# Optimization experiments

Measured on AMD Instinct MI355X. Metric: run time of the kernel, lower is better.

Reference implementation:

```python
import jax, jax.numpy as jnp
import numpy as np

N = 20000      # total nodes
E = 320000     # edges (before self loops)
B = 8          # graphs in batch
F_IN = 100
HID = 256
HEADS = 4
DIMS = [(256, 256), (256, 128), (128, 64), (64, 32)]  # (in_dim, out_dim) per level
NEG_SLOPE = 0.2
LN_EPS = 1e-5


def _glorot(k, shape):
    fan = shape[0] + shape[-1]
    return jax.random.normal(k, shape, jnp.float32) * jnp.sqrt(2.0 / fan)


def setup_inputs() -> dict:
    key = jax.random.key(0)
    ks = jax.random.split(key, 32)
    inp = {}
    inp["x"] = jax.random.normal(ks[0], (N, F_IN), jnp.float32)
    inp["edge_index"] = jax.random.randint(ks[1], (2, E), 0, N)
    inp["batch"] = jnp.sort(jax.random.randint(ks[2], (N,), 0, B))
    inp["W_in"] = _glorot(ks[3], (F_IN, HID))
    inp["b_in"] = jnp.zeros((HID,), jnp.float32)
    i = 4
    for l, (di, do) in enumerate(DIMS):
        inp[f"W{l}"] = _glorot(ks[i], (di, HEADS * do)); i += 1
        inp[f"as{l}"] = _glorot(ks[i], (HEADS, do)); i += 1
        inp[f"ad{l}"] = _glorot(ks[i], (HEADS, do)); i += 1
        inp[f"b{l}"] = jnp.zeros((do,), jnp.float32)
        inp[f"g{l}"] = jnp.ones((do,), jnp.float32)
        inp[f"be{l}"] = jnp.zeros((do,), jnp.float32)
    inp["W_out"] = _glorot(ks[i], (DIMS[-1][1], 1))
    inp["b_out"] = jnp.zeros((1,), jnp.float32)
    return inp


def _gat(x, src, dst, W, a_s, a_d, b):
    # PyG GATConv, heads=HEADS, concat=False (head mean), bias after mean
    h = (x @ W).reshape(N, HEADS, -1)              # [N,H,C]
    al_s = (h * a_s).sum(-1)                        # [N,H]
    al_d = (h * a_d).sum(-1)                        # [N,H]
    e = jax.nn.leaky_relu(al_s[src] + al_d[dst], NEG_SLOPE)  # [Etot,H]
    m = jax.ops.segment_max(e, dst, num_segments=N)
    m = jnp.where(jnp.isfinite(m), m, 0.0)
    ex = jnp.exp(e - m[dst])
    den = jax.ops.segment_sum(ex, dst, num_segments=N)
    alpha = ex / (den[dst] + 1e-16)                 # segment softmax over incoming edges
    out = jax.ops.segment_sum(alpha[:, :, None] * h[src], dst, num_segments=N)
    return out.mean(axis=1) + b                     # [N,C]


def _ln(x, g, b):
    mu = x.mean(-1, keepdims=True)
    var = ((x - mu) ** 2).mean(-1, keepdims=True)
    return (x - mu) * jax.lax.rsqrt(var + LN_EPS) * g + b


def _forward(x, edge_index, batch, W_in, b_in, level_params, W_out, b_out):
    loop = jnp.arange(N)
    src = jnp.concatenate([edge_index[0], loop])    # add self loops (GATConv default)
    dst = jnp.concatenate([edge_index[1], loop])
    h = jax.nn.relu(x @ W_in + b_in)
    for (di, do), (W, a_s, a_d, b, g, be) in zip(DIMS, level_params):
        out = _gat(h, src, dst, W, a_s, a_d, b)
        out = jax.nn.relu(out)
        out = _ln(out, g, be)
        # dropout is identity in eval mode
        if di == do:
            out = out + h
        h = out
    cnt = jax.ops.segment_sum(jnp.ones((N,), h.dtype), batch, num_segments=B)
    pooled = jax.ops.segment_sum(h, batch, num_segments=B) / jnp.maximum(cnt, 1.0)[:, None]
    return (pooled @ W_out + b_out)[:, 0]           # [B]


def reference(x, edge_index, batch, W_in, b_in,
              W0, as0, ad0, b0, g0, be0,
              W1, as1, ad1, b1, g1, be1,
              W2, as2, ad2, b2, g2, be2,
              W3, as3, ad3, b3, g3, be3,
              W_out, b_out):
    level_params = [
        (W0, as0, ad0, b0, g0, be0),
        (W1, as1, ad1, b1, g1, be1),
        (W2, as2, ad2, b2, g2, be2),
        (W3, as3, ad3, b3, g3, be3),
    ]
    return _forward(x, edge_index, batch, W_in, b_in, level_params, W_out, b_out)
```

## Files before the change

kernel.cpp:

```cpp
#include <hip/hip_runtime.h>
#include <hip/hip_bf16.h>
#include <cstdint>

constexpr int NN   = 20000;
constexpr int NE   = 320000;
constexpr int ETOT = NE + NN;
constexpr int BG   = 8;
constexpr int FIN  = 100;
constexpr int HID  = 256;
constexpr int H    = 4;
constexpr float SLOPE  = 0.2f;
constexpr float LN_EPS = 1e-5f;

#define DEVFN __device__ __forceinline__

typedef __bf16 bf16x8 __attribute__((ext_vector_type(8)));
typedef float  f32x4  __attribute__((ext_vector_type(4)));
typedef float  f32x2  __attribute__((ext_vector_type(2)));

DEVFN float lrelu(float v) { return v > 0.f ? v : SLOPE * v; }
DEVFN ushort f2bf(float f) {
    unsigned u = __float_as_uint(f);
    return (ushort)((u + 0x7fffu + ((u >> 16) & 1u)) >> 16);
}
DEVFN float bf_lo(unsigned u) { return __uint_as_float(u << 16); }
DEVFN float bf_hi(unsigned u) { return __uint_as_float(u & 0xffff0000u); }
DEVFN float bf2f(unsigned u) { return __uint_as_float(u << 16); }

__global__ void zero_u32(uint32_t* __restrict__ p, int n) {
    int i = blockIdx.x * blockDim.x + threadIdx.x;
    if (i < n) p[i] = 0u;
}

__global__ void count_deg(const int* __restrict__ ei, int* __restrict__ deg) {
    int k = blockIdx.x * blockDim.x + threadIdx.x;
    if (k >= ETOT) return;
    int d = (k < NE) ? ei[NE + k] : (k - NE);
    atomicAdd(&deg[d], 1);
}

__global__ void scan_kernel(const int* __restrict__ deg, int* __restrict__ rowptr) {
    __shared__ int buf[1024];
    int carry = 0;
    for (int base = 0; base < NN; base += 1024) {
        int i = base + threadIdx.x;
        int v = (i < NN) ? deg[i] : 0;
        buf[threadIdx.x] = v;
        __syncthreads();
        for (int off = 1; off < 1024; off <<= 1) {
            int t = (threadIdx.x >= off) ? buf[threadIdx.x - off] : 0;
            __syncthreads();
            buf[threadIdx.x] += t;
            __syncthreads();
        }
        int incl = buf[threadIdx.x];
        if (i < NN) rowptr[i] = carry + incl - v;
        int total = buf[1023];
        __syncthreads();
        carry += total;
    }
    if (threadIdx.x == 0) rowptr[NN] = carry;
}

__global__ void scatter_edges(const int* __restrict__ ei, const int* __restrict__ rowptr,
                              int* __restrict__ fill, int* __restrict__ esrc) {
    int k = blockIdx.x * blockDim.x + threadIdx.x;
    if (k >= ETOT) return;
    int s, d;
    if (k < NE) { s = ei[k]; d = ei[NE + k]; }
    else        { s = k - NE; d = k - NE; }
    int pos = rowptr[d] + atomicAdd(&fill[d], 1);
    esrc[pos] = s;
}

constexpr int CXN  = NN * 128;
constexpr int CWI  = 256 * 128;
constexpr int CW0  = 1024 * 256;
constexpr int CW1  = 512 * 256;
constexpr int CW2  = 256 * 128;
constexpr int CW3  = 128 * 64;
constexpr int CTOT = CXN + CWI + CW0 + CW1 + CW2 + CW3;

__global__ void conv_all(const float* __restrict__ x, const float* __restrict__ Wi,
                         const float* __restrict__ W0, const float* __restrict__ W1,
                         const float* __restrict__ W2, const float* __restrict__ W3,
                         ushort* __restrict__ xpad, ushort* __restrict__ wti,
                         ushort* __restrict__ wt0, ushort* __restrict__ wt1,
                         ushort* __restrict__ wt2, ushort* __restrict__ wt3) {
    int id = blockIdx.x * blockDim.x + threadIdx.x;
    if (id < CXN) {
        int n = id >> 7, k = id & 127;
        xpad[id] = (k < FIN) ? f2bf(x[(size_t)n * FIN + k]) : (ushort)0;
        return;
    }
    id -= CXN;
    if (id < CWI) { int n = id / 128, k = id - n * 128;
        wti[id] = (k < FIN) ? f2bf(Wi[(size_t)k * 256 + n]) : (ushort)0; return; }
    id -= CWI;
    if (id < CW0) { int n = id / 256, k = id - n * 256;
        wt0[id] = f2bf(W0[(size_t)k * 1024 + n]); return; }
    id -= CW0;
    if (id < CW1) { int n = id / 256, k = id - n * 256;
        wt1[id] = f2bf(W1[(size_t)k * 512 + n]); return; }
    id -= CW1;
    if (id < CW2) { int n = id / 128, k = id - n * 128;
        wt2[id] = f2bf(W2[(size_t)k * 256 + n]); return; }
    id -= CW2;
    if (id < CW3) { int n = id / 64, k = id - n * 64;
        wt3[id] = f2bf(W3[(size_t)k * 128 + n]); return; }
}

template <int K, int NC, bool BR, bool AL>
__launch_bounds__(256)
__global__ void gemm_mfma(const ushort* __restrict__ A, const ushort* __restrict__ Wt,
                          const float* __restrict__ bias, void* __restrict__ Cout,
                          const float* __restrict__ a_s, const float* __restrict__ a_d,
                          float* __restrict__ al_s, float* __restrict__ al_d, int M) {
    constexpr int LDK = K + 8;
    constexpr int DO_AL = NC / H;
    __shared__ ushort As[64 * LDK];
    __shared__ ushort Bs[64 * LDK];
    const int row0 = blockIdx.x * 64;
    const int col0 = blockIdx.y * 64;
    const int tid = threadIdx.x;
    constexpr int CH = K / 8;
    for (int c = tid; c < 64 * CH; c += 256) {
        int r = c / CH, cc = c - r * CH;
        int gr = row0 + r;
        uint4 v = make_uint4(0u, 0u, 0u, 0u);
        if (gr < M) v = *(const uint4*)(A + (size_t)gr * K + cc * 8);
        *(uint4*)(&As[r * LDK + cc * 8]) = v;
        uint4 w = *(const uint4*)(Wt + (size_t)(col0 + r) * K + cc * 8);
        *(uint4*)(&Bs[r * LDK + cc * 8]) = w;
    }
    __syncthreads();
    const int wave = tid >> 6;
    const int lane = tid & 63;
    const int m = lane & 15;
    const int q = lane >> 4;
    f32x4 acc0 = {0.f, 0.f, 0.f, 0.f}, acc1 = acc0, acc2 = acc0, acc3 = acc0;
    const ushort* ap  = &As[(wave * 16 + m) * LDK + q * 8];
    const ushort* bp0 = &Bs[(0 * 16 + m) * LDK + q * 8];
    const ushort* bp1 = &Bs[(1 * 16 + m) * LDK + q * 8];
    const ushort* bp2 = &Bs[(2 * 16 + m) * LDK + q * 8];
    const ushort* bp3 = &Bs[(3 * 16 + m) * LDK + q * 8];
#pragma unroll
    for (int kk = 0; kk < K / 32; kk++) {
        bf16x8 a = *(const bf16x8*)(ap + kk * 32);
        acc0 = __builtin_amdgcn_mfma_f32_16x16x32_bf16(a, *(const bf16x8*)(bp0 + kk * 32), acc0, 0, 0, 0);
        acc1 = __builtin_amdgcn_mfma_f32_16x16x32_bf16(a, *(const bf16x8*)(bp1 + kk * 32), acc1, 0, 0, 0);
        acc2 = __builtin_amdgcn_mfma_f32_16x16x32_bf16(a, *(const bf16x8*)(bp2 + kk * 32), acc2, 0, 0, 0);
        acc3 = __builtin_amdgcn_mfma_f32_16x16x32_bf16(a, *(const bf16x8*)(bp3 + kk * 32), acc3, 0, 0, 0);
    }
    const int grow0 = row0 + wave * 16 + q * 4;
    if (!AL) {
        ushort* Cb = (ushort*)Cout + (size_t)grow0 * NC + col0 + m;
        float b0 = 0, b1 = 0, b2 = 0, b3 = 0;
        if (BR) {
            b0 = bias[col0 + m];      b1 = bias[col0 + m + 16];
            b2 = bias[col0 + m + 32]; b3 = bias[col0 + m + 48];
        }
#pragma unroll
        for (int r = 0; r < 4; r++) {
            if (grow0 + r < M) {
                float v0 = acc0[r], v1 = acc1[r], v2 = acc2[r], v3 = acc3[r];
                if (BR) {
                    v0 = fmaxf(v0 + b0, 0.f); v1 = fmaxf(v1 + b1, 0.f);
                    v2 = fmaxf(v2 + b2, 0.f); v3 = fmaxf(v3 + b3, 0.f);
                }
                Cb[(size_t)r * NC + 0]  = f2bf(v0);
                Cb[(size_t)r * NC + 16] = f2bf(v1);
                Cb[(size_t)r * NC + 32] = f2bf(v2);
                Cb[(size_t)r * NC + 48] = f2bf(v3);
            }
        }
    } else {
        uchar* Cb = (uchar*)Cout + (size_t)grow0 * NC + col0 + m;
#pragma unroll
        for (int r = 0; r < 4; r++) {
            if (grow0 + r < M) {
                int pk01 = __builtin_amdgcn_cvt_pk_fp8_f32(acc0[r], acc1[r], 0, false);
                int pk23 = __builtin_amdgcn_cvt_pk_fp8_f32(acc2[r], acc3[r], 0, false);
                Cb[(size_t)r * NC + 0]  = (uchar)(pk01 & 0xff);
                Cb[(size_t)r * NC + 16] = (uchar)((pk01 >> 8) & 0xff);
                Cb[(size_t)r * NC + 32] = (uchar)(pk23 & 0xff);
                Cb[(size_t)r * NC + 48] = (uchar)((pk23 >> 8) & 0xff);
            }
        }
        float asv[4], adv[4];
#pragma unroll
        for (int t = 0; t < 4; t++) {
            int gc = col0 + m + 16 * t;
            asv[t] = a_s[gc];
            adv[t] = a_d[gc];
        }
        const int h_lo = col0 / DO_AL;
        const int h_hi = (col0 + 32) / DO_AL;
#pragma unroll
        for (int r = 0; r < 4; r++) {
            float ps0 = acc0[r] * asv[0] + acc1[r] * asv[1];
            float ps1 = acc2[r] * asv[2] + acc3[r] * asv[3];
            float pd0 = acc0[r] * adv[0] + acc1[r] * adv[1];
            float pd1 = acc2[r] * adv[2] + acc3[r] * adv[3];
#pragma unroll
            for (int off = 1; off < 16; off <<= 1) {
                ps0 += __shfl_xor(ps0, off);
                ps1 += __shfl_xor(ps1, off);
                pd0 += __shfl_xor(pd0, off);
                pd1 += __shfl_xor(pd1, off);
            }
            if (m == 0 && grow0 + r < M) {
                if (h_lo == h_hi) {
                    atomicAdd(&al_s[(grow0 + r) * H + h_lo], ps0 + ps1);
                    atomicAdd(&al_d[(grow0 + r) * H + h_lo], pd0 + pd1);
                } else {
                    atomicAdd(&al_s[(grow0 + r) * H + h_lo], ps0);
                    atomicAdd(&al_s[(grow0 + r) * H + h_hi], ps1);
                    atomicAdd(&al_d[(grow0 + r) * H + h_lo], pd0);
                    atomicAdd(&al_d[(grow0 + r) * H + h_hi], pd1);
                }
            }
        }
    }
}

__global__ void softmax_csr(const int* __restrict__ rowptr, const int* __restrict__ esrc,
                            const float* __restrict__ al_s, const float* __restrict__ al_d,
                            float4* __restrict__ alpha) {
    int wid = (blockIdx.x * blockDim.x + threadIdx.x) >> 6;
    int lane = threadIdx.x & 63;
    if (wid >= NN) return;
    int p0 = rowptr[wid], p1 = rowptr[wid + 1];
    float4 d4 = ((const float4*)al_d)[wid];
    float m0 = -1e30f, m1 = -1e30f, m2 = -1e30f, m3 = -1e30f;
    for (int p = p0 + lane; p < p1; p += 64) {
        int s = esrc[p];
        float4 s4 = ((const float4*)al_s)[s];
        m0 = fmaxf(m0, lrelu(s4.x + d4.x));
        m1 = fmaxf(m1, lrelu(s4.y + d4.y));
        m2 = fmaxf(m2, lrelu(s4.z + d4.z));
        m3 = fmaxf(m3, lrelu(s4.w + d4.w));
    }
#pragma unroll
    for (int off = 32; off > 0; off >>= 1) {
        m0 = fmaxf(m0, __shfl_xor(m0, off));
        m1 = fmaxf(m1, __shfl_xor(m1, off));
        m2 = fmaxf(m2, __shfl_xor(m2, off));
        m3 = fmaxf(m3, __shfl_xor(m3, off));
    }
    float s0 = 0.f, s1 = 0.f, s2 = 0.f, s3 = 0.f;
    for (int p = p0 + lane; p < p1; p += 64) {
        int s = esrc[p];
        float4 s4 = ((const float4*)al_s)[s];
        s0 += __expf(lrelu(s4.x + d4.x) - m0);
        s1 += __expf(lrelu(s4.y + d4.y) - m1);
        s2 += __expf(lrelu(s4.z + d4.z) - m2);
        s3 += __expf(lrelu(s4.w + d4.w) - m3);
    }
#pragma unroll
    for (int off = 32; off > 0; off >>= 1) {
        s0 += __shfl_xor(s0, off);
        s1 += __shfl_xor(s1, off);
        s2 += __shfl_xor(s2, off);
        s3 += __shfl_xor(s3, off);
    }
    float i0 = 0.25f / (s0 + 1e-16f), i1 = 0.25f / (s1 + 1e-16f);
    float i2 = 0.25f / (s2 + 1e-16f), i3 = 0.25f / (s3 + 1e-16f);
    for (int p = p0 + lane; p < p1; p += 64) {
        int s = esrc[p];
        float4 s4 = ((const float4*)al_s)[s];
        alpha[p] = make_float4(__expf(lrelu(s4.x + d4.x) - m0) * i0,
                               __expf(lrelu(s4.y + d4.y) - m1) * i1,
                               __expf(lrelu(s4.z + d4.z) - m2) * i2,
                               __expf(lrelu(s4.w + d4.w) - m3) * i3);
    }
}

template <int DO, bool RESID>
__launch_bounds__(256)
__global__ void aggregate(const uchar* __restrict__ hproj, const int* __restrict__ rowptr,
                          const int* __restrict__ esrc, const float4* __restrict__ alpha,
                          const float* __restrict__ bias, const float* __restrict__ gamma,
                          const float* __restrict__ beta, const ushort* __restrict__ hprev,
                          ushort* __restrict__ hout) {
    constexpr int HDO = H * DO;
    constexpr int SL  = HDO / 16;
    constexpr int EPI = 64 / SL;
    constexpr int HL  = DO / 16;
    const int wave = threadIdx.x >> 6;
    const int lane = threadIdx.x & 63;
    const int n = blockIdx.x * 4 + wave;
    const int e  = lane / SL;
    const int sl = lane - e * SL;
    const int hsel = sl / HL;
    const int p0 = rowptr[n], p1 = rowptr[n + 1];
    const uint4* hp4 = (const uint4*)hproj;

    float acc[16];
#pragma unroll
    for (int j = 0; j < 16; j++) acc[j] = 0.f;

    int p = p0 + e;
    bool valid = p < p1;
    float a = 0.f;
    uint4 v = make_uint4(0, 0, 0, 0);
    if (valid) {
        int src = esrc[p];
        float4 al = alpha[p];
        a = (hsel == 0) ? al.x : (hsel == 1) ? al.y : (hsel == 2) ? al.z : al.w;
        v = hp4[(size_t)src * SL + sl];
    }
    while (__any(valid)) {
        int pn = p + EPI;
        bool vn = valid && (pn < p1);
        float an = 0.f;
        uint4 vnx = make_uint4(0, 0, 0, 0);
        if (vn) {
            int srcn = esrc[pn];
            float4 al = alpha[pn];
            an = (hsel == 0) ? al.x : (hsel == 1) ? al.y : (hsel == 2) ? al.z : al.w;
            vnx = hp4[(size_t)srcn * SL + sl];
        }
        if (valid) {
            f32x2 d;
            d = __builtin_amdgcn_cvt_pk_f32_fp8(v.x, false); acc[0]  += a * d[0]; acc[1]  += a * d[1];
            d = __builtin_amdgcn_cvt_pk_f32_fp8(v.x, true);  acc[2]  += a * d[0]; acc[3]  += a * d[1];
            d = __builtin_amdgcn_cvt_pk_f32_fp8(v.y, false); acc[4]  += a * d[0]; acc[5]  += a * d[1];
            d = __builtin_amdgcn_cvt_pk_f32_fp8(v.y, true);  acc[6]  += a * d[0]; acc[7]  += a * d[1];
            d = __builtin_amdgcn_cvt_pk_f32_fp8(v.z, false); acc[8]  += a * d[0]; acc[9]  += a * d[1];
            d = __builtin_amdgcn_cvt_pk_f32_fp8(v.z, true);  acc[10] += a * d[0]; acc[11] += a * d[1];
            d = __builtin_amdgcn_cvt_pk_f32_fp8(v.w, false); acc[12] += a * d[0]; acc[13] += a * d[1];
            d = __builtin_amdgcn_cvt_pk_f32_fp8(v.w, true);  acc[14] += a * d[0]; acc[15] += a * d[1];
        }
        p = pn; valid = vn; a = an; v = vnx;
    }

#pragma unroll
    for (int off = 32; off >= HL; off >>= 1) {
#pragma unroll
        for (int j = 0; j < 16; j++) acc[j] += __shfl_xor(acc[j], off);
    }
    const int c2 = lane & (HL - 1);
    const int cb = c2 * 16;
    float val[16];
    float s = 0.f;
    {
        float4 b0 = *(const float4*)(bias + cb);
        float4 b1 = *(const float4*)(bias + cb + 4);
        float4 b2 = *(const float4*)(bias + cb + 8);
        float4 b3 = *(const float4*)(bias + cb + 12);
        float bb[16] = {b0.x, b0.y, b0.z, b0.w, b1.x, b1.y, b1.z, b1.w,
                        b2.x, b2.y, b2.z, b2.w, b3.x, b3.y, b3.z, b3.w};
#pragma unroll
        for (int j = 0; j < 16; j++) {
            val[j] = fmaxf(acc[j] + bb[j], 0.f);
            s += val[j];
        }
    }
#pragma unroll
    for (int off = 1; off < HL; off <<= 1) s += __shfl_xor(s, off);
    float mu = s / DO;
    float q = 0.f;
#pragma unroll
    for (int j = 0; j < 16; j++) {
        val[j] -= mu;
        q += val[j] * val[j];
    }
#pragma unroll
    for (int off = 1; off < HL; off <<= 1) q += __shfl_xor(q, off);
    float rstd = rsqrtf(q / DO + LN_EPS);

    if (lane < HL) {
        float4 g0 = *(const float4*)(gamma + cb);
        float4 g1 = *(const float4*)(gamma + cb + 4);
        float4 g2 = *(const float4*)(gamma + cb + 8);
        float4 g3 = *(const float4*)(gamma + cb + 12);
        float4 e0 = *(const float4*)(beta + cb);
        float4 e1 = *(const float4*)(beta + cb + 4);
        float4 e2 = *(const float4*)(beta + cb + 8);
        float4 e3 = *(const float4*)(beta + cb + 12);
        float gg[16] = {g0.x, g0.y, g0.z, g0.w, g1.x, g1.y, g1.z, g1.w,
                        g2.x, g2.y, g2.z, g2.w, g3.x, g3.y, g3.z, g3.w};
        float ee[16] = {e0.x, e0.y, e0.z, e0.w, e1.x, e1.y, e1.z, e1.w,
                        e2.x, e2.y, e2.z, e2.w, e3.x, e3.y, e3.z, e3.w};
        float o[16];
#pragma unroll
        for (int j = 0; j < 16; j++) o[j] = val[j] * rstd * gg[j] + ee[j];
        if (RESID) {
            const uint4* pv = (const uint4*)(hprev + (size_t)n * DO + cb);
            uint4 r0 = pv[0], r1 = pv[1];
            unsigned rr[8] = {r0.x, r0.y, r0.z, r0.w, r1.x, r1.y, r1.z, r1.w};
#pragma unroll
            for (int j = 0; j < 8; j++) {
                o[2 * j]     += bf_lo(rr[j]);
                o[2 * j + 1] += bf_hi(rr[j]);
            }
        }
        unsigned w[8];
#pragma unroll
        for (int j = 0; j < 8; j++)
            w[j] = (unsigned)f2bf(o[2 * j]) | ((unsigned)f2bf(o[2 * j + 1]) << 16);
        uint4* op = (uint4*)(hout + (size_t)n * DO + cb);
        op[0] = make_uint4(w[0], w[1], w[2], w[3]);
        op[1] = make_uint4(w[4], w[5], w[6], w[7]);
    }
}

__global__ void pool_accum2(const ushort* __restrict__ h, const int* __restrict__ batch,
                            float* __restrict__ pooled, float* __restrict__ cnt) {
    __shared__ float lp[BG * 32];
    __shared__ float lc[BG];
    for (int i = threadIdx.x; i < BG * 32; i += blockDim.x) lp[i] = 0.f;
    if (threadIdx.x < BG) lc[threadIdx.x] = 0.f;
    __syncthreads();
    int c = threadIdx.x & 31;
    int rb = threadIdx.x >> 5;
    for (int n = blockIdx.x * 8 + rb; n < NN; n += gridDim.x * 8) {
        int b = batch[n];
        atomicAdd(&lp[b * 32 + c], bf2f((unsigned)h[(size_t)n * 32 + c]));
        if (c == 0) atomicAdd(&lc[b], 1.f);
    }
    __syncthreads();
    for (int i = threadIdx.x; i < BG * 32; i += blockDim.x) atomicAdd(&pooled[i], lp[i]);
    if (threadIdx.x < BG) atomicAdd(&cnt[threadIdx.x], lc[threadIdx.x]);
}

__global__ void final_out(const float* __restrict__ pooled, const float* __restrict__ cnt,
                          const float* __restrict__ Wo, const float* __restrict__ bo,
                          float* __restrict__ out) {
    int b = threadIdx.x;
    if (b < BG) {
        float inv = 1.f / fmaxf(cnt[b], 1.f);
        float acc = 0.f;
        for (int c = 0; c < 32; c++) acc += pooled[b * 32 + c] * inv * Wo[c];
        out[b] = acc + bo[0];
    }
}

extern "C" void kernel_launch(void* const* d_in, const int* in_sizes, int n_in,
                              void* d_out, int out_size, void* d_ws, size_t ws_size,
                              hipStream_t stream) {
    const float* x     = (const float*)d_in[0];
    const int*   ei    = (const int*)d_in[1];
    const int*   batch = (const int*)d_in[2];
    const float* Wi    = (const float*)d_in[3];
    const float* bi    = (const float*)d_in[4];
    const float* Wl[4]  = {(const float*)d_in[5],  (const float*)d_in[11], (const float*)d_in[17], (const float*)d_in[23]};
    const float* Asl[4] = {(const float*)d_in[6],  (const float*)d_in[12], (const float*)d_in[18], (const float*)d_in[24]};
    const float* Adl[4] = {(const float*)d_in[7],  (const float*)d_in[13], (const float*)d_in[19], (const float*)d_in[25]};
    const float* Bl[4]  = {(const float*)d_in[8],  (const float*)d_in[14], (const float*)d_in[20], (const float*)d_in[26]};
    const float* Gl[4]  = {(const float*)d_in[9],  (const float*)d_in[15], (const float*)d_in[21], (const float*)d_in[27]};
    const float* Bel[4] = {(const float*)d_in[10], (const float*)d_in[16], (const float*)d_in[22], (const float*)d_in[28]};
    const float* Wo = (const float*)d_in[29];
    const float* bo = (const float*)d_in[30];

    char* p = (char*)d_ws;
    auto take = [&](size_t bytes) -> void* {
        void* r = (void*)p;
        p += (bytes + 255) & ~(size_t)255;
        return r;
    };
    ushort*   hAbf   = (ushort*)take((size_t)NN * HID * 2);
    ushort*   hBbf   = (ushort*)take((size_t)NN * HID * 2);
    uchar*    hproj  = (uchar*)take((size_t)NN * H * HID);
    ushort*   xpad   = (ushort*)take((size_t)NN * 128 * 2);
    int*      rowptr = (int*)take((size_t)(NN + 1) * 4);
    int*      esrc   = (int*)take((size_t)ETOT * 4);
    float4*   alpha  = (float4*)take((size_t)ETOT * 16);
    ushort*   wti    = (ushort*)take((size_t)CWI * 2);
    ushort*   wt0    = (ushort*)take((size_t)CW0 * 2);
    ushort*   wt1    = (ushort*)take((size_t)CW1 * 2);
    ushort*   wt2    = (ushort*)take((size_t)CW2 * 2);
    ushort*   wt3    = (ushort*)take((size_t)CW3 * 2);
    char*     zbase  = p;
    int*      deg    = (int*)take((size_t)NN * 4);
    int*      fill   = (int*)take((size_t)NN * 4);
    float*    pooled = (float*)take((size_t)BG * 32 * 4);
    float*    cnt    = (float*)take((size_t)BG * 4);
    float*    als[4], *ald[4];
    for (int l = 0; l < 4; l++) {
        als[l] = (float*)take((size_t)NN * H * 4);
        ald[l] = (float*)take((size_t)NN * H * 4);
    }
    const int zcount = (int)((p - zbase) / 4);
    (void)ws_size; (void)n_in; (void)in_sizes; (void)out_size;

    const int ZB = 256;
    const int egrid = (ETOT + ZB - 1) / ZB;
    const int mtiles = (NN + 63) / 64;
    const int sgrid = (NN * 64 + 255) / 256;
    const int agrid = NN / 4;

    zero_u32<<<(zcount + ZB - 1) / ZB, ZB, 0, stream>>>((uint32_t*)zbase, zcount);
    conv_all<<<(CTOT + ZB - 1) / ZB, ZB, 0, stream>>>(x, Wi, Wl[0], Wl[1], Wl[2], Wl[3],
                                                      xpad, wti, wt0, wt1, wt2, wt3);
    count_deg<<<egrid, ZB, 0, stream>>>(ei, deg);
    scan_kernel<<<1, 1024, 0, stream>>>(deg, rowptr);
    scatter_edges<<<egrid, ZB, 0, stream>>>(ei, rowptr, fill, esrc);

    gemm_mfma<128, 256, true, false><<<dim3(mtiles, 4), 256, 0, stream>>>(
        xpad, wti, bi, hAbf, nullptr, nullptr, nullptr, nullptr, NN);

    gemm_mfma<256, 1024, false, true><<<dim3(mtiles, 16), 256, 0, stream>>>(
        hAbf, wt0, nullptr, hproj, Asl[0], Adl[0], als[0], ald[0], NN);
    softmax_csr<<<sgrid, 256, 0, stream>>>(rowptr, esrc, als[0], ald[0], alpha);
    aggregate<256, true><<<agrid, 256, 0, stream>>>(hproj, rowptr, esrc, alpha,
                                                    Bl[0], Gl[0], Bel[0], hAbf, hBbf);
    gemm_mfma<256, 512, false, true><<<dim3(mtiles, 8), 256, 0, stream>>>(
        hBbf, wt1, nullptr, hproj, Asl[1], Adl[1], als[1], ald[1], NN);
    softmax_csr<<<sgrid, 256, 0, stream>>>(rowptr, esrc, als[1], ald[1], alpha);
    aggregate<128, false><<<agrid, 256, 0, stream>>>(hproj, rowptr, esrc, alpha,
                                                     Bl[1], Gl[1], Bel[1], nullptr, hAbf);
    gemm_mfma<128, 256, false, true><<<dim3(mtiles, 4), 256, 0, stream>>>(
        hAbf, wt2, nullptr, hproj, Asl[2], Adl[2], als[2], ald[2], NN);
    softmax_csr<<<sgrid, 256, 0, stream>>>(rowptr, esrc, als[2], ald[2], alpha);
    aggregate<64, false><<<agrid, 256, 0, stream>>>(hproj, rowptr, esrc, alpha,
                                                    Bl[2], Gl[2], Bel[2], nullptr, hBbf);
    gemm_mfma<64, 128, false, true><<<dim3(mtiles, 2), 256, 0, stream>>>(
        hBbf, wt3, nullptr, hproj, Asl[3], Adl[3], als[3], ald[3], NN);
    softmax_csr<<<sgrid, 256, 0, stream>>>(rowptr, esrc, als[3], ald[3], alpha);
    aggregate<32, false><<<agrid, 256, 0, stream>>>(hproj, rowptr, esrc, alpha,
                                                    Bl[3], Gl[3], Bel[3], nullptr, hAbf);

    pool_accum2<<<80, 256, 0, stream>>>(hAbf, batch, pooled, cnt);
    final_out<<<1, 64, 0, stream>>>(pooled, cnt, Wo, bo, (float*)d_out);
}
```

Measured before the change: 580.1 us.

## Reuse A tile across column tiles, warp-shuffle scan, and unroll aggregate gather

The GEMM now loads the A row tile into LDS once and loops over several 64-column weight tiles per block, cutting redundant A reads and shrinking the grid. The single-block scan replaces its LDS Hillis-Steele loop, which needed many barriers, with wave shuffle scans. The aggregate kernel keeps two edges in flight per iteration and uses packed f32x2 FMAs to raise memory-level parallelism. Fewer GEMM blocks may underfill the GPU on the smaller layers, and the extra per-tile barriers serialize the weight loads.

Measured after the change: 574.5 us. No clear change (-1.0%).

```diff
diff --git a/kernel.cpp b/kernel.cpp
--- a/kernel.cpp
+++ b/kernel.cpp
@@ -40,24 +40,38 @@
 }
 
 __global__ void scan_kernel(const int* __restrict__ deg, int* __restrict__ rowptr) {
-    __shared__ int buf[1024];
+    __shared__ int wsum[16];
+    __shared__ int woff[16];
+    __shared__ int ctot;
+    const int lane = threadIdx.x & 63;
+    const int wv   = threadIdx.x >> 6;
     int carry = 0;
     for (int base = 0; base < NN; base += 1024) {
         int i = base + threadIdx.x;
         int v = (i < NN) ? deg[i] : 0;
-        buf[threadIdx.x] = v;
+        int s = v;
+#pragma unroll
+        for (int off = 1; off < 64; off <<= 1) {
+            int t = __shfl_up(s, off);
+            if (lane >= off) s += t;
+        }
+        if (lane == 63) wsum[wv] = s;
         __syncthreads();
-        for (int off = 1; off < 1024; off <<= 1) {
-            int t = (threadIdx.x >= off) ? buf[threadIdx.x - off] : 0;
-            __syncthreads();
-            buf[threadIdx.x] += t;
-            __syncthreads();
-        }
-        int incl = buf[threadIdx.x];
-        if (i < NN) rowptr[i] = carry + incl - v;
-        int total = buf[1023];
+        if (wv == 0 && lane < 16) {
+            int ws = wsum[lane];
+            int sc = ws;
+#pragma unroll
+            for (int off = 1; off < 16; off <<= 1) {
+                int t = __shfl_up(sc, off);
+                if (lane >= off) sc += t;
+            }
+            woff[lane] = sc - ws;
+            if (lane == 15) ctot = sc;
+        }
         __syncthreads();
-        carry += total;
+        if (i < NN) rowptr[i] = carry + woff[wv] + (s - v);
+        carry += ctot;
+        __syncthreads();
     }
     if (threadIdx.x == 0) rowptr[NN] = carry;
 }
@@ -110,7 +124,7 @@
         wt3[id] = f2bf(W3[(size_t)k * 128 + n]); return; }
 }
 
-template <int K, int NC, bool BR, bool AL>
+template <int K, int NC, int CT, bool BR, bool AL>
 __launch_bounds__(256)
 __global__ void gemm_mfma(const ushort* __restrict__ A, const ushort* __restrict__ Wt,
                           const float* __restrict__ bias, void* __restrict__ Cout,
@@ -121,7 +135,7 @@
     __shared__ ushort As[64 * LDK];
     __shared__ ushort Bs[64 * LDK];
     const int row0 = blockIdx.x * 64;
-    const int col0 = blockIdx.y * 64;
+    const int colbase = blockIdx.y * (64 * CT);
     const int tid = threadIdx.x;
     constexpr int CH = K / 8;
     for (int c = tid; c < 64 * CH; c += 256) {
@@ -130,97 +144,105 @@
         uint4 v = make_uint4(0u, 0u, 0u, 0u);
         if (gr < M) v = *(const uint4*)(A + (size_t)gr * K + cc * 8);
         *(uint4*)(&As[r * LDK + cc * 8]) = v;
-        uint4 w = *(const uint4*)(Wt + (size_t)(col0 + r) * K + cc * 8);
-        *(uint4*)(&Bs[r * LDK + cc * 8]) = w;
-    }
-    __syncthreads();
+    }
     const int wave = tid >> 6;
     const int lane = tid & 63;
     const int m = lane & 15;
     const int q = lane >> 4;
-    f32x4 acc0 = {0.f, 0.f, 0.f, 0.f}, acc1 = acc0, acc2 = acc0, acc3 = acc0;
     const ushort* ap  = &As[(wave * 16 + m) * LDK + q * 8];
     const ushort* bp0 = &Bs[(0 * 16 + m) * LDK + q * 8];
     const ushort* bp1 = &Bs[(1 * 16 + m) * LDK + q * 8];
     const ushort* bp2 = &Bs[(2 * 16 + m) * LDK + q * 8];
     const ushort* bp3 = &Bs[(3 * 16 + m) * LDK + q * 8];
-#pragma unroll
-    for (int kk = 0; kk < K / 32; kk++) {
-        bf16x8 a = *(const bf16x8*)(ap + kk * 32);
-        acc0 = __builtin_amdgcn_mfma_f32_16x16x32_bf16(a, *(const bf16x8*)(bp0 + kk * 32), acc0, 0, 0, 0);
-        acc1 = __builtin_amdgcn_mfma_f32_16x16x32_bf16(a, *(const bf16x8*)(bp1 + kk * 32), acc1, 0, 0, 0);
-        acc2 = __builtin_amdgcn_mfma_f32_16x16x32_bf16(a, *(const bf16x8*)(bp2 + kk * 32), acc2, 0, 0, 0);
-        acc3 = __builtin_amdgcn_mfma_f32_16x16x32_bf16(a, *(const bf16x8*)(bp3 + kk * 32), acc3, 0, 0, 0);
-    }
     const int grow0 = row0 + wave * 16 + q * 4;
-    if (!AL) {
-        ushort* Cb = (ushort*)Cout + (size_t)grow0 * NC + col0 + m;
-        float b0 = 0, b1 = 0, b2 = 0, b3 = 0;
-        if (BR) {
-            b0 = bias[col0 + m];      b1 = bias[col0 + m + 16];
-            b2 = bias[col0 + m + 32]; b3 = bias[col0 + m + 48];
-        }
-#pragma unroll
-        for (int r = 0; r < 4; r++) {
-            if (grow0 + r < M) {
-                float v0 = acc0[r], v1 = acc1[r], v2 = acc2[r], v3 = acc3[r];
-                if (BR) {
-                    v0 = fmaxf(v0 + b0, 0.f); v1 = fmaxf(v1 + b1, 0.f);
-                    v2 = fmaxf(v2 + b2, 0.f); v3 = fmaxf(v3 + b3, 0.f);
+
+    for (int ct = 0; ct < CT; ct++) {
+        const int col0 = colbase + ct * 64;
+        for (int c = tid; c < 64 * CH; c += 256) {
+            int r = c / CH, cc = c - r * CH;
+            *(uint4*)(&Bs[r * LDK + cc * 8]) =
+                *(const uint4*)(Wt + (size_t)(col0 + r) * K + cc * 8);
+        }
+        __syncthreads();
+        f32x4 acc0 = {0.f, 0.f, 0.f, 0.f}, acc1 = acc0, acc2 = acc0, acc3 = acc0;
+#pragma unroll
+        for (int kk = 0; kk < K / 32; kk++) {
+            bf16x8 a = *(const bf16x8*)(ap + kk * 32);
+            acc0 = __builtin_amdgcn_mfma_f32_16x16x32_bf16(a, *(const bf16x8*)(bp0 + kk * 32), acc0, 0, 0, 0);
+            acc1 = __builtin_amdgcn_mfma_f32_16x16x32_bf16(a, *(const bf16x8*)(bp1 + kk * 32), acc1, 0, 0, 0);
+            acc2 = __builtin_amdgcn_mfma_f32_16x16x32_bf16(a, *(const bf16x8*)(bp2 + kk * 32), acc2, 0, 0, 0);
+            acc3 = __builtin_amdgcn_mfma_f32_16x16x32_bf16(a, *(const bf16x8*)(bp3 + kk * 32), acc3, 0, 0, 0);
+        }
+        if (!AL) {
+            ushort* Cb = (ushort*)Cout + (size_t)grow0 * NC + col0 + m;
+            float b0 = 0, b1 = 0, b2 = 0, b3 = 0;
+            if (BR) {
+                b0 = bias[col0 + m];      b1 = bias[col0 + m + 16];
+                b2 = bias[col0 + m + 32]; b3 = bias[col0 + m + 48];
+            }
+#pragma unroll
+            for (int r = 0; r < 4; r++) {
+                if (grow0 + r < M) {
+                    float v0 = acc0[r], v1 = acc1[r], v2 = acc2[r], v3 = acc3[r];
+                    if (BR) {
+                        v0 = fmaxf(v0 + b0, 0.f); v1 = fmaxf(v1 + b1, 0.f);
+                        v2 = fmaxf(v2 + b2, 0.f); v3 = fmaxf(v3 + b3, 0.f);
+                    }
+                    Cb[(size_t)r * NC + 0]  = f2bf(v0);
+                    Cb[(size_t)r * NC + 16] = f2bf(v1);
+                    Cb[(size_t)r * NC + 32] = f2bf(v2);
+                    Cb[(size_t)r * NC + 48] = f2bf(v3);
                 }
-                Cb[(size_t)r * NC + 0]  = f2bf(v0);
-                Cb[(size_t)r * NC + 16] = f2bf(v1);
-                Cb[(size_t)r * NC + 32] = f2bf(v2);
-                Cb[(size_t)r * NC + 48] = f2bf(v3);
-            }
-        }
-    } else {
-        uchar* Cb = (uchar*)Cout + (size_t)grow0 * NC + col0 + m;
-#pragma unroll
-        for (int r = 0; r < 4; r++) {
-            if (grow0 + r < M) {
-                int pk01 = __builtin_amdgcn_cvt_pk_fp8_f32(acc0[r], acc1[r], 0, false);
-                int pk23 = __builtin_amdgcn_cvt_pk_fp8_f32(acc2[r], acc3[r], 0, false);
-                Cb[(size_t)r * NC + 0]  = (uchar)(pk01 & 0xff);
-                Cb[(size_t)r * NC + 16] = (uchar)((pk01 >> 8) & 0xff);
-                Cb[(size_t)r * NC + 32] = (uchar)(pk23 & 0xff);
-                Cb[(size_t)r * NC + 48] = (uchar)((pk23 >> 8) & 0xff);
-            }
-        }
-        float asv[4], adv[4];
-#pragma unroll
-        for (int t = 0; t < 4; t++) {
-            int gc = col0 + m + 16 * t;
-            asv[t] = a_s[gc];
-            adv[t] = a_d[gc];
-        }
-        const int h_lo = col0 / DO_AL;
-        const int h_hi = (col0 + 32) / DO_AL;
-#pragma unroll
-        for (int r = 0; r < 4; r++) {
-            float ps0 = acc0[r] * asv[0] + acc1[r] * asv[1];
-            float ps1 = acc2[r] * asv[2] + acc3[r] * asv[3];
-            float pd0 = acc0[r] * adv[0] + acc1[r] * adv[1];
-            float pd1 = acc2[r] * adv[2] + acc3[r] * adv[3];
-#pragma unroll
-            for (int off = 1; off < 16; off <<= 1) {
-                ps0 += __shfl_xor(ps0, off);
-                ps1 += __shfl_xor(ps1, off);
-                pd0 += __shfl_xor(pd0, off);
-                pd1 += __shfl_xor(pd1, off);
-            }
-            if (m == 0 && grow0 + r < M) {
-                if (h_lo == h_hi) {
-                    atomicAdd(&al_s[(grow0 + r) * H + h_lo], ps0 + ps1);
-                    atomicAdd(&al_d[(grow0 + r) * H + h_lo], pd0 + pd1);
-                } else {
-                    atomicAdd(&al_s[(grow0 + r) * H + h_lo], ps0);
-                    atomicAdd(&al_s[(grow0 + r) * H + h_hi], ps1);
-                    atomicAdd(&al_d[(grow0 + r) * H + h_lo], pd0);
-                    atomicAdd(&al_d[(grow0 + r) * H + h_hi], pd1);
+            }
+        } else {
+            uchar* Cb = (uchar*)Cout + (size_t)grow0 * NC + col0 + m;
+#pragma unroll
+            for (int r = 0; r < 4; r++) {
+                if (grow0 + r < M) {
+                    int pk01 = __builtin_amdgcn_cvt_pk_fp8_f32(acc0[r], acc1[r], 0, false);
+                    int pk23 = __builtin_amdgcn_cvt_pk_fp8_f32(acc2[r], acc3[r], 0, false);
+                    Cb[(size_t)r * NC + 0]  = (uchar)(pk01 & 0xff);
+                    Cb[(size_t)r * NC + 16] = (uchar)((pk01 >> 8) & 0xff);
+                    Cb[(size_t)r * NC + 32] = (uchar)(pk23 & 0xff);
+                    Cb[(size_t)r * NC + 48] = (uchar)((pk23 >> 8) & 0xff);
                 }
             }
-        }
+            float asv[4], adv[4];
+#pragma unroll
+            for (int t = 0; t < 4; t++) {
+                int gc = col0 + m + 16 * t;
+                asv[t] = a_s[gc];
+                adv[t] = a_d[gc];
+            }
+            const int h_lo = col0 / DO_AL;
+            const int h_hi = (col0 + 32) / DO_AL;
+#pragma unroll
+            for (int r = 0; r < 4; r++) {
+                float ps0 = acc0[r] * asv[0] + acc1[r] * asv[1];
+                float ps1 = acc2[r] * asv[2] + acc3[r] * asv[3];
+                float pd0 = acc0[r] * adv[0] + acc1[r] * adv[1];
+                float pd1 = acc2[r] * adv[2] + acc3[r] * adv[3];
+#pragma unroll
+                for (int off = 1; off < 16; off <<= 1) {
+                    ps0 += __shfl_xor(ps0, off);
+                    ps1 += __shfl_xor(ps1, off);
+                    pd0 += __shfl_xor(pd0, off);
+                    pd1 += __shfl_xor(pd1, off);
+                }
+                if (m == 0 && grow0 + r < M) {
+                    if (h_lo == h_hi) {
+                        atomicAdd(&al_s[(grow0 + r) * H + h_lo], ps0 + ps1);
+                        atomicAdd(&al_d[(grow0 + r) * H + h_lo], pd0 + pd1);
+                    } else {
+                        atomicAdd(&al_s[(grow0 + r) * H + h_lo], ps0);
+                        atomicAdd(&al_s[(grow0 + r) * H + h_hi], ps1);
+                        atomicAdd(&al_d[(grow0 + r) * H + h_lo], pd0);
+                        atomicAdd(&al_d[(grow0 + r) * H + h_hi], pd1);
+                    }
+                }
+            }
+        }
+        __syncthreads();
     }
 }
 
@@ -296,44 +318,48 @@
     const int p0 = rowptr[n], p1 = rowptr[n + 1];
     const uint4* hp4 = (const uint4*)hproj;
 
+    f32x2 acc2[8];
+#pragma unroll
+    for (int j = 0; j < 8; j++) acc2[j] = f32x2{0.f, 0.f};
+
+    auto sel = [&](float4 al) {
+        return (hsel == 0) ? al.x : (hsel == 1) ? al.y : (hsel == 2) ? al.z : al.w;
+    };
+    auto consume = [&](uint4 v, float a) {
+        f32x2 ap = {a, a};
+        acc2[0] += ap * __builtin_amdgcn_cvt_pk_f32_fp8(v.x, false);
+        acc2[1] += ap * __builtin_amdgcn_cvt_pk_f32_fp8(v.x, true);
+        acc2[2] += ap * __builtin_amdgcn_cvt_pk_f32_fp8(v.y, false);
+        acc2[3] += ap * __builtin_amdgcn_cvt_pk_f32_fp8(v.y, true);
+        acc2[4] += ap * __builtin_amdgcn_cvt_pk_f32_fp8(v.z, false);
+        acc2[5] += ap * __builtin_amdgcn_cvt_pk_f32_fp8(v.z, true);
+        acc2[6] += ap * __builtin_amdgcn_cvt_pk_f32_fp8(v.w, false);
+        acc2[7] += ap * __builtin_amdgcn_cvt_pk_f32_fp8(v.w, true);
+    };
+
+    int p = p0 + e;
+    bool va = p < p1;
+    bool vb = (p + EPI) < p1;
+    float aa = 0.f, ab = 0.f;
+    uint4 ua = make_uint4(0, 0, 0, 0), ub = make_uint4(0, 0, 0, 0);
+    if (va) { aa = sel(alpha[p]);       ua = hp4[(size_t)esrc[p] * SL + sl]; }
+    if (vb) { ab = sel(alpha[p + EPI]); ub = hp4[(size_t)esrc[p + EPI] * SL + sl]; }
+
+    while (__any(va)) {
+        int pa = p + 2 * EPI, pb = p + 3 * EPI;
+        bool va2 = pa < p1, vb2 = pb < p1;
+        float aa2 = 0.f, ab2 = 0.f;
+        uint4 ua2 = make_uint4(0, 0, 0, 0), ub2 = make_uint4(0, 0, 0, 0);
+        if (va2) { aa2 = sel(alpha[pa]); ua2 = hp4[(size_t)esrc[pa] * SL + sl]; }
+        if (vb2) { ab2 = sel(alpha[pb]); ub2 = hp4[(size_t)esrc[pb] * SL + sl]; }
+        if (va) consume(ua, aa);
+        if (vb) consume(ub, ab);
+        p = pa; va = va2; vb = vb2; aa = aa2; ab = ab2; ua = ua2; ub = ub2;
+    }
+
     float acc[16];
 #pragma unroll
-    for (int j = 0; j < 16; j++) acc[j] = 0.f;
-
-    int p = p0 + e;
-    bool valid = p < p1;
-    float a = 0.f;
-    uint4 v = make_uint4(0, 0, 0, 0);
-    if (valid) {
-        int src = esrc[p];
-        float4 al = alpha[p];
-        a = (hsel == 0) ? al.x : (hsel == 1) ? al.y : (hsel == 2) ? al.z : al.w;
-        v = hp4[(size_t)src * SL + sl];
-    }
-    while (__any(valid)) {
-        int pn = p + EPI;
-        bool vn = valid && (pn < p1);
-        float an = 0.f;
-        uint4 vnx = make_uint4(0, 0, 0, 0);
-        if (vn) {
-            int srcn = esrc[pn];
-            float4 al = alpha[pn];
-            an = (hsel == 0) ? al.x : (hsel == 1) ? al.y : (hsel == 2) ? al.z : al.w;
-            vnx = hp4[(size_t)srcn * SL + sl];
-        }
-        if (valid) {
-            f32x2 d;
-            d = __builtin_amdgcn_cvt_pk_f32_fp8(v.x, false); acc[0]  += a * d[0]; acc[1]  += a * d[1];
-            d = __builtin_amdgcn_cvt_pk_f32_fp8(v.x, true);  acc[2]  += a * d[0]; acc[3]  += a * d[1];
-            d = __builtin_amdgcn_cvt_pk_f32_fp8(v.y, false); acc[4]  += a * d[0]; acc[5]  += a * d[1];
-            d = __builtin_amdgcn_cvt_pk_f32_fp8(v.y, true);  acc[6]  += a * d[0]; acc[7]  += a * d[1];
-            d = __builtin_amdgcn_cvt_pk_f32_fp8(v.z, false); acc[8]  += a * d[0]; acc[9]  += a * d[1];
-            d = __builtin_amdgcn_cvt_pk_f32_fp8(v.z, true);  acc[10] += a * d[0]; acc[11] += a * d[1];
-            d = __builtin_amdgcn_cvt_pk_f32_fp8(v.w, false); acc[12] += a * d[0]; acc[13] += a * d[1];
-            d = __builtin_amdgcn_cvt_pk_f32_fp8(v.w, true);  acc[14] += a * d[0]; acc[15] += a * d[1];
-        }
-        p = pn; valid = vn; a = an; v = vnx;
-    }
+    for (int j = 0; j < 8; j++) { acc[2 * j] = acc2[j][0]; acc[2 * j + 1] = acc2[j][1]; }
 
 #pragma unroll
     for (int off = 32; off >= HL; off >>= 1) {
@@ -498,25 +524,25 @@
     scan_kernel<<<1, 1024, 0, stream>>>(deg, rowptr);
     scatter_edges<<<egrid, ZB, 0, stream>>>(ei, rowptr, fill, esrc);
 
-    gemm_mfma<128, 256, true, false><<<dim3(mtiles, 4), 256, 0, stream>>>(
+    gemm_mfma<128, 256, 2, true, false><<<dim3(mtiles, 2), 256, 0, stream>>>(
         xpad, wti, bi, hAbf, nullptr, nullptr, nullptr, nullptr, NN);
 
-    gemm_mfma<256, 1024, false, true><<<dim3(mtiles, 16), 256, 0, stream>>>(
+    gemm_mfma<256, 1024, 4, false, true><<<dim3(mtiles, 4), 256, 0, stream>>>(
         hAbf, wt0, nullptr, hproj, Asl[0], Adl[0], als[0], ald[0], NN);
     softmax_csr<<<sgrid, 256, 0, stream>>>(rowptr, esrc, als[0], ald[0], alpha);
     aggregate<256, true><<<agrid, 256, 0, stream>>>(hproj, rowptr, esrc, alpha,
                                                     Bl[0], Gl[0], Bel[0], hAbf, hBbf);
-    gemm_mfma<256, 512, false, true><<<dim3(mtiles, 8), 256, 0, stream>>>(
+    gemm_mfma<256, 512, 4, false, true><<<dim3(mtiles, 2), 256, 0, stream>>>(
         hBbf, wt1, nullptr, hproj, Asl[1], Adl[1], als[1], ald[1], NN);
     softmax_csr<<<sgrid, 256, 0, stream>>>(rowptr, esrc, als[1], ald[1], alpha);
     aggregate<128, false><<<agrid, 256, 0, stream>>>(hproj, rowptr, esrc, alpha,
                                                      Bl[1], Gl[1], Bel[1], nullptr, hAbf);
-    gemm_mfma<128, 256, false, true><<<dim3(mtiles, 4), 256, 0, stream>>>(
+    gemm_mfma<128, 256, 4, false, true><<<dim3(mtiles, 1), 256, 0, stream>>>(
         hAbf, wt2, nullptr, hproj, Asl[2], Adl[2], als[2], ald[2], NN);
     softmax_csr<<<sgrid, 256, 0, stream>>>(rowptr, esrc, als[2], ald[2], alpha);
     aggregate<64, false><<<agrid, 256, 0, stream>>>(hproj, rowptr, esrc, alpha,
                                                     Bl[2], Gl[2], Bel[2], nullptr, hBbf);
-    gemm_mfma<64, 128, false, true><<<dim3(mtiles, 2), 256, 0, stream>>>(
+    gemm_mfma<64, 128, 2, false, true><<<dim3(mtiles, 1), 256, 0, stream>>>(
         hBbf, wt3, nullptr, hproj, Asl[3], Adl[3], als[3], ald[3], NN);
     softmax_csr<<<sgrid, 256, 0, stream>>>(rowptr, esrc, als[3], ald[3], alpha);
     aggregate<32, false><<<agrid, 256, 0, stream>>>(hproj, rowptr, esrc, alpha,
```
